# Kernel tuning notes

Hardware: AMD Instinct MI355X
Metric: run time of the kernel (lower is better)

The kernel has to match this reference:

```python
import jax, jax.numpy as jnp
import numpy as np

D, H, N, BS = 3072, 2048, 16, 512
MAX_LATENT_VAR = 0.1


def setup_inputs() -> dict:
    key = jax.random.key(0)
    ks = jax.random.split(key, 12)
    s = 0.02
    return {
        "x": jax.random.normal(ks[0], (BS, D), dtype=jnp.float32),
        "eps": jax.random.normal(ks[1], (1, BS, N), dtype=jnp.float32),
        "enc_W1": jax.random.normal(ks[2], (D, H), dtype=jnp.float32) * s,
        "enc_b1": jnp.zeros((H,), dtype=jnp.float32),
        "enc_Wmu": jax.random.normal(ks[3], (H, N), dtype=jnp.float32) * s,
        "enc_bmu": jnp.zeros((N,), dtype=jnp.float32),
        "enc_Wls": jax.random.normal(ks[4], (H, 1), dtype=jnp.float32) * s,
        "enc_bls": jnp.zeros((1,), dtype=jnp.float32),
        "dec_W1": jax.random.normal(ks[5], (N, H), dtype=jnp.float32) * 0.1,
        "dec_b1": jnp.zeros((H,), dtype=jnp.float32),
        "dec_W2": jax.random.normal(ks[6], (H, D), dtype=jnp.float32) * s,
        "dec_b2": jnp.zeros((D,), dtype=jnp.float32),
    }


def reference(x, eps, enc_W1, enc_b1, enc_Wmu, enc_bmu, enc_Wls, enc_bls,
              dec_W1, dec_b1, dec_W2, dec_b2):
    bs, Dd = x.shape
    n = dec_W1.shape[0]

    def dec(z):  # smooth 2-layer MLP decoder (supports nested autodiff)
        return jnp.tanh(z @ dec_W1 + dec_b1) @ dec_W2 + dec_b2

    # encoder.forward_with_sigma
    h = jnp.tanh(x @ enc_W1 + enc_b1)
    z_star = h @ enc_Wmu + enc_bmu                      # (bs, n)
    sigma = jnp.exp(h @ enc_Wls + enc_bls)[:, 0]        # (bs,)

    # per-sample Jacobian of decoder: (bs, D, n)
    J = jax.vmap(jax.jacfwd(dec))(z_star)

    # per-sample Hessian of f(z) = stop_grad(d) . d,  d = (x - dec(z)) / sigma
    def f_hess(z, xi, sg):
        d = (xi - dec(z)) / sg
        return jnp.dot(jax.lax.stop_gradient(d), d)
    hess = jax.vmap(jax.hessian(f_hess), in_axes=(0, 0, 0))(z_star, x, sigma)  # (bs,n,n)

    eye = jnp.eye(n, dtype=x.dtype)
    Prec = jnp.einsum('bdi,bdj->bij', J, J) / (sigma ** 2)[:, None, None] + eye + hess

    eigvals = jnp.linalg.eigvalsh(Prec)                 # ascending, (bs, n)
    eigmin = eigvals[:, 0]
    delta = 1.0 / MAX_LATENT_VAR - eigmin               # (bs,)
    Prec = Prec + eye * delta[:, None, None]
    eigvals = eigvals + delta[:, None]

    # upper-triangular Cholesky: U^T U = Prec
    U = jnp.swapaxes(jnp.linalg.cholesky(Prec), -1, -2)  # (bs, n, n)

    def solve1(u, e):  # solve U y = e
        return jax.scipy.linalg.solve_triangular(u, e[:, None], lower=False)[:, 0]
    z_off = jax.vmap(jax.vmap(solve1, in_axes=(0, 0)), in_axes=(None, 0))(U, eps)  # (ne,bs,n)
    z_sample = z_star[None] + z_off

    n_eval = eps.shape[0]
    recon = dec(z_sample.reshape(-1, n)).reshape(n_eval, bs, Dd)
    recon_loss = ((recon - x[None]) ** 2).sum(axis=2).mean(axis=0) / (2.0 * sigma ** 2)
    latent_energy = (z_star ** 2).sum(axis=1) / 2.0 + (1.0 / eigvals).sum(axis=1) / 2.0
    logdet_loss = jnp.log(eigvals).sum(axis=1) / 2.0
    sigma_loss = Dd * jnp.log(sigma)
    neg_log_prob = (recon_loss + latent_energy + logdet_loss + sigma_loss) / Dd
    return (neg_log_prob, recon_loss, latent_energy, logdet_loss, sigma)
```

## Files before the change

kernel.cpp:

```cpp
#include <hip/hip_runtime.h>
#include <hip/hip_bf16.h>
#include <math.h>

#define D_ 3072
#define H_ 2048
#define N_ 16
#define BS_ 512

typedef short s16x8 __attribute__((ext_vector_type(8)));
typedef float f32x4v __attribute__((ext_vector_type(4)));
typedef __hip_bfloat16 bf16;

__device__ __forceinline__ void gload_lds16(const void* g, void* l) {
    __builtin_amdgcn_global_load_lds((const __attribute__((address_space(1))) void*)g,
                                     (__attribute__((address_space(3))) void*)l, 16, 0, 0);
}

__device__ __forceinline__ float bf2f(unsigned short u) {
    unsigned v = (unsigned)u << 16; float f; __builtin_memcpy(&f, &v, 4); return f;
}

__global__ __launch_bounds__(256) void mfma_nt_slab(
    const bf16* __restrict__ A, const bf16* __restrict__ Bt,
    float* __restrict__ C, int M, int N, int K, int KC)
{
    __shared__ __align__(16) bf16 As[128 * 32];
    __shared__ __align__(16) bf16 Bs[128 * 32];
    const int tid = threadIdx.x;
    const int w = tid >> 6, l = tid & 63;
    const int wr = w >> 1, wc = w & 1;
    const int m0 = blockIdx.y * 128, n0 = blockIdx.x * 128;
    const int kbeg = blockIdx.z * KC;
    float* Cz = C + (size_t)blockIdx.z * M * N;

    f32x4v acc[4][4];
    #pragma unroll
    for (int a = 0; a < 4; ++a)
        #pragma unroll
        for (int b = 0; b < 4; ++b) acc[a][b] = (f32x4v){0.f, 0.f, 0.f, 0.f};

    const int srow = l >> 2;
    const int scol = (l & 3) * 8;

    for (int k0 = kbeg; k0 < kbeg + KC; k0 += 32) {
        #pragma unroll
        for (int q = 0; q < 2; ++q) {
            int r0 = w * 32 + q * 16;
            gload_lds16(&A[(size_t)(m0 + r0 + srow) * K + k0 + scol], &As[r0 * 32]);
            gload_lds16(&Bt[(size_t)(n0 + r0 + srow) * K + k0 + scol], &Bs[r0 * 32]);
        }
        __syncthreads();
        s16x8 af[4], bfr[4];
        #pragma unroll
        for (int mf = 0; mf < 4; ++mf)
            af[mf] = *(const s16x8*)&As[(wr * 64 + mf * 16 + (l & 15)) * 32 + (l >> 4) * 8];
        #pragma unroll
        for (int nf = 0; nf < 4; ++nf)
            bfr[nf] = *(const s16x8*)&Bs[(wc * 64 + nf * 16 + (l & 15)) * 32 + (l >> 4) * 8];
        #pragma unroll
        for (int mf = 0; mf < 4; ++mf)
            #pragma unroll
            for (int nf = 0; nf < 4; ++nf)
                acc[mf][nf] = __builtin_amdgcn_mfma_f32_16x16x32_bf16(af[mf], bfr[nf], acc[mf][nf], 0, 0, 0);
        __syncthreads();
    }

    #pragma unroll
    for (int mf = 0; mf < 4; ++mf)
        #pragma unroll
        for (int nf = 0; nf < 4; ++nf) {
            int n = n0 + wc * 64 + nf * 16 + (l & 15);
            #pragma unroll
            for (int r = 0; r < 4; ++r) {
                int m = m0 + wr * 64 + mf * 16 + (l >> 4) * 4 + r;
                Cz[(size_t)m * N + n] = acc[mf][nf][r];
            }
        }
}

__global__ __launch_bounds__(256) void mfma_nt_sk(
    const bf16* __restrict__ A, const bf16* __restrict__ Bt,
    float* __restrict__ C, int M, int N, int K, int KC)
{
    __shared__ __align__(16) bf16 As[128 * 32];
    __shared__ __align__(16) bf16 Bs[128 * 32];
    const int tid = threadIdx.x;
    const int w = tid >> 6, l = tid & 63;
    const int wr = w >> 1, wc = w & 1;
    const int m0 = blockIdx.y * 128, n0 = blockIdx.x * 128;
    const int kbeg = blockIdx.z * KC;

    f32x4v acc[4][4];
    #pragma unroll
    for (int a = 0; a < 4; ++a)
        #pragma unroll
        for (int b = 0; b < 4; ++b) acc[a][b] = (f32x4v){0.f, 0.f, 0.f, 0.f};

    const int srow = l >> 2;
    const int scol = (l & 3) * 8;

    for (int k0 = kbeg; k0 < kbeg + KC; k0 += 32) {
        #pragma unroll
        for (int q = 0; q < 2; ++q) {
            int r0 = w * 32 + q * 16;
            gload_lds16(&A[(size_t)(m0 + r0 + srow) * K + k0 + scol], &As[r0 * 32]);
            gload_lds16(&Bt[(size_t)(n0 + r0 + srow) * K + k0 + scol], &Bs[r0 * 32]);
        }
        __syncthreads();
        s16x8 af[4], bfr[4];
        #pragma unroll
        for (int mf = 0; mf < 4; ++mf)
            af[mf] = *(const s16x8*)&As[(wr * 64 + mf * 16 + (l & 15)) * 32 + (l >> 4) * 8];
        #pragma unroll
        for (int nf = 0; nf < 4; ++nf)
            bfr[nf] = *(const s16x8*)&Bs[(wc * 64 + nf * 16 + (l & 15)) * 32 + (l >> 4) * 8];
        #pragma unroll
        for (int mf = 0; mf < 4; ++mf)
            #pragma unroll
            for (int nf = 0; nf < 4; ++nf)
                acc[mf][nf] = __builtin_amdgcn_mfma_f32_16x16x32_bf16(af[mf], bfr[nf], acc[mf][nf], 0, 0, 0);
        __syncthreads();
    }

    #pragma unroll
    for (int mf = 0; mf < 4; ++mf)
        #pragma unroll
        for (int nf = 0; nf < 4; ++nf) {
            int n = n0 + wc * 64 + nf * 16 + (l & 15);
            #pragma unroll
            for (int r = 0; r < 4; ++r) {
                int m = m0 + wr * 64 + mf * 16 + (l >> 4) * 4 + r;
                atomicAdd(&C[(size_t)m * N + n], acc[mf][nf][r]);
            }
        }
}

__global__ __launch_bounds__(256) void ep_ebf(const float* __restrict__ C4,
    const float* __restrict__ bias, const float* __restrict__ X,
    bf16* __restrict__ Eout, int MN, int N)
{
    const size_t SL = (size_t)MN;
    int base = (blockIdx.x * 256 + threadIdx.x) * 8;
    if (base < MN) {
        float4 c0 = *(const float4*)&C4[base];
        float4 c1 = *(const float4*)&C4[base + 4];
        float4 d0 = *(const float4*)&C4[SL + base];
        float4 d1 = *(const float4*)&C4[SL + base + 4];
        float4 e0 = *(const float4*)&C4[2*SL + base];
        float4 e1 = *(const float4*)&C4[2*SL + base + 4];
        float4 f0 = *(const float4*)&C4[3*SL + base];
        float4 f1 = *(const float4*)&C4[3*SL + base + 4];
        float4 x0 = *(const float4*)&X[base];
        float4 x1 = *(const float4*)&X[base + 4];
        int n = base % N;
        float4 b0 = *(const float4*)&bias[n];
        float4 b1 = *(const float4*)&bias[n + 4];
        union { s16x8 v; bf16 e[8]; } u;
        u.e[0] = __float2bfloat16(x0.x - (c0.x + d0.x + e0.x + f0.x + b0.x));
        u.e[1] = __float2bfloat16(x0.y - (c0.y + d0.y + e0.y + f0.y + b0.y));
        u.e[2] = __float2bfloat16(x0.z - (c0.z + d0.z + e0.z + f0.z + b0.z));
        u.e[3] = __float2bfloat16(x0.w - (c0.w + d0.w + e0.w + f0.w + b0.w));
        u.e[4] = __float2bfloat16(x1.x - (c1.x + d1.x + e1.x + f1.x + b1.x));
        u.e[5] = __float2bfloat16(x1.y - (c1.y + d1.y + e1.y + f1.y + b1.y));
        u.e[6] = __float2bfloat16(x1.z - (c1.z + d1.z + e1.z + f1.z + b1.z));
        u.e[7] = __float2bfloat16(x1.w - (c1.w + d1.w + e1.w + f1.w + b1.w));
        *(s16x8*)&Eout[base] = u.v;
    }
}

__global__ __launch_bounds__(256) void ep_recon_fin(const float* __restrict__ C4,
    const float* __restrict__ bias, const float* __restrict__ X,
    const float* __restrict__ sigma, const float* __restrict__ lsig, float* __restrict__ d_out)
{
    const size_t SL = (size_t)BS_ * D_;
    int m = blockIdx.x;
    float s = 0.f;
    for (int n = threadIdx.x * 4; n < D_; n += 1024) {
        size_t i = (size_t)m * D_ + n;
        float4 c0 = *(const float4*)&C4[i];
        float4 c1 = *(const float4*)&C4[SL + i];
        float4 c2 = *(const float4*)&C4[2*SL + i];
        float4 c3 = *(const float4*)&C4[3*SL + i];
        float4 bb = *(const float4*)&bias[n];
        float4 xx = *(const float4*)&X[i];
        float v0 = c0.x + c1.x + c2.x + c3.x + bb.x - xx.x;
        float v1 = c0.y + c1.y + c2.y + c3.y + bb.y - xx.y;
        float v2 = c0.z + c1.z + c2.z + c3.z + bb.z - xx.z;
        float v3 = c0.w + c1.w + c2.w + c3.w + bb.w - xx.w;
        s += v0 * v0 + v1 * v1 + v2 * v2 + v3 * v3;
    }
    __shared__ float red[4];
    int wid = threadIdx.x >> 6, lane = threadIdx.x & 63;
    #pragma unroll
    for (int off = 32; off; off >>= 1) s += __shfl_xor(s, off);
    if (lane == 0) red[wid] = s;
    __syncthreads();
    if (threadIdx.x == 0) {
        float tot = red[0] + red[1] + red[2] + red[3];
        float sg = sigma[m];
        float rl = tot / (2.0f * sg * sg);
        float le = d_out[2 * 512 + m];
        float ld = d_out[3 * 512 + m];
        d_out[m] = (rl + le + ld) / 3072.0f + lsig[m];
        d_out[512 + m] = rl;
    }
}

__global__ __launch_bounds__(256) void jtj_fused(
    const bf16* __restrict__ Vt, const bf16* __restrict__ W2t,
    float* __restrict__ S, int Mb, int b0)
{
    __shared__ union {
        struct { __align__(16) bf16 As[3][128 * 32]; __align__(16) bf16 Bs[3][128 * 32]; } s;
        __align__(16) bf16 J[128 * 136];
    } u;
    const int tid = threadIdx.x;
    const int w = tid >> 6, l = tid & 63;
    const int wr = w >> 1, wc = w & 1;

    int mb, nbk;
    if ((Mb & 7) == 0) {
        int lin = blockIdx.y * 24 + blockIdx.x;
        int xcd = lin & 7, idx = lin >> 3;
        int mchunk = Mb >> 3;
        mb = xcd * mchunk + idx / 24;
        nbk = idx % 24;
    } else { mb = blockIdx.y; nbk = blockIdx.x; }
    const int m0 = mb * 128, n0 = nbk * 128;

    f32x4v acc[4][4];
    #pragma unroll
    for (int a = 0; a < 4; ++a)
        #pragma unroll
        for (int b = 0; b < 4; ++b) acc[a][b] = (f32x4v){0.f, 0.f, 0.f, 0.f};

    const int strow = tid >> 2;
    const int scb = (((tid & 3) ^ ((tid >> 3) & 3)) << 4);

    auto STAGE = [&](int kt, int bi) {
        const char* a0 = (const char*)Vt  + ((size_t)(m0 + strow) * H_ + kt * 32) * 2 + scb;
        const char* b0p = (const char*)W2t + ((size_t)(n0 + strow) * H_ + kt * 32) * 2 + scb;
        char* la = (char*)u.s.As[bi] + w * 1024;
        char* lb = (char*)u.s.Bs[bi] + w * 1024;
        gload_lds16(a0, la);
        gload_lds16(a0 + (size_t)64 * H_ * 2, la + 4096);
        gload_lds16(b0p, lb);
        gload_lds16(b0p + (size_t)64 * H_ * 2, lb + 4096);
    };

    STAGE(0, 0);
    STAGE(1, 1);

    const int rdcb = (((l >> 4) ^ ((l >> 1) & 3)) << 4);

    for (int kt = 0; kt < H_ / 32; ++kt) {
        __builtin_amdgcn_sched_barrier(0);
        if (kt == H_ / 32 - 1) asm volatile("s_waitcnt vmcnt(0)" ::: "memory");
        else                   asm volatile("s_waitcnt vmcnt(4)" ::: "memory");
        __builtin_amdgcn_s_barrier();
        __builtin_amdgcn_sched_barrier(0);
        const int cur = kt % 3;
        const char* Ab = (const char*)u.s.As[cur];
        const char* Bb = (const char*)u.s.Bs[cur];
        s16x8 af[4], bfr[4];
        #pragma unroll
        for (int mf = 0; mf < 4; ++mf)
            af[mf] = *(const s16x8*)(Ab + (wr * 64 + mf * 16 + (l & 15)) * 64 + rdcb);
        #pragma unroll
        for (int nf = 0; nf < 4; ++nf)
            bfr[nf] = *(const s16x8*)(Bb + (wc * 64 + nf * 16 + (l & 15)) * 64 + rdcb);
        if (kt + 2 < H_ / 32) STAGE(kt + 2, (kt + 2) % 3);
        #pragma unroll
        for (int mf = 0; mf < 4; ++mf)
            #pragma unroll
            for (int nf = 0; nf < 4; ++nf)
                acc[mf][nf] = __builtin_amdgcn_mfma_f32_16x16x32_bf16(af[mf], bfr[nf], acc[mf][nf], 0, 0, 0);
    }

    __syncthreads();
    #pragma unroll
    for (int mf = 0; mf < 4; ++mf) {
        int rbase = wr * 64 + mf * 16 + (l >> 4) * 4;
        #pragma unroll
        for (int nf = 0; nf < 4; ++nf) {
            int col = wc * 64 + nf * 16 + (l & 15);
            #pragma unroll
            for (int r = 0; r < 4; ++r)
                u.J[(rbase + r) * 136 + col] = __float2bfloat16(acc[mf][nf][r]);
        }
    }
    __syncthreads();

    #pragma unroll
    for (int t2 = 0; t2 < 2; ++t2) {
        int bl = w * 2 + t2;
        f32x4v sp = (f32x4v){0.f, 0.f, 0.f, 0.f};
        #pragma unroll
        for (int kq = 0; kq < 4; ++kq) {
            s16x8 fr = *(const s16x8*)&u.J[(bl * 16 + (l & 15)) * 136 + kq * 32 + (l >> 4) * 8];
            sp = __builtin_amdgcn_mfma_f32_16x16x32_bf16(fr, fr, sp, 0, 0, 0);
        }
        int bglob = b0 + mb * 8 + bl;
        #pragma unroll
        for (int r = 0; r < 4; ++r)
            atomicAdd(&S[(size_t)bglob * 256 + ((l >> 4) * 4 + r) * 16 + (l & 15)], sp[r]);
    }
}

__global__ __launch_bounds__(256) void hess_mfma(const float* __restrict__ t,
    const float* __restrict__ g, const bf16* __restrict__ W1b, float* __restrict__ S)
{
    const int w = threadIdx.x >> 6, l = threadIdx.x & 63;
    const int b = blockIdx.x * 4 + w;
    const int row = l & 15, kq = (l >> 4) * 8;

    f32x4v sp = (f32x4v){0.f, 0.f, 0.f, 0.f};
    for (int k0 = 0; k0 < H_; k0 += 32) {
        int kk = k0 + kq;
        s16x8 wf = *(const s16x8*)&W1b[(size_t)row * H_ + kk];
        float4 t0 = *(const float4*)&t[(size_t)b * H_ + kk];
        float4 t1 = *(const float4*)&t[(size_t)b * H_ + kk + 4];
        float4 g0 = *(const float4*)&g[(size_t)b * H_ + kk];
        float4 g1 = *(const float4*)&g[(size_t)b * H_ + kk + 4];
        float wv[8];
        wv[0] = 2.f * g0.x * t0.x * (1.f - t0.x * t0.x);
        wv[1] = 2.f * g0.y * t0.y * (1.f - t0.y * t0.y);
        wv[2] = 2.f * g0.z * t0.z * (1.f - t0.z * t0.z);
        wv[3] = 2.f * g0.w * t0.w * (1.f - t0.w * t0.w);
        wv[4] = 2.f * g1.x * t1.x * (1.f - t1.x * t1.x);
        wv[5] = 2.f * g1.y * t1.y * (1.f - t1.y * t1.y);
        wv[6] = 2.f * g1.z * t1.z * (1.f - t1.z * t1.z);
        wv[7] = 2.f * g1.w * t1.w * (1.f - t1.w * t1.w);
        union { s16x8 v; bf16 e[8]; } af;
        #pragma unroll
        for (int e = 0; e < 8; ++e)
            af.e[e] = __float2bfloat16(wv[e] * bf2f((unsigned short)wf[e]));
        sp = __builtin_amdgcn_mfma_f32_16x16x32_bf16(af.v, wf, sp, 0, 0, 0);
    }
    #pragma unroll
    for (int r = 0; r < 4; ++r)
        S[(size_t)b * 256 + ((l >> 4) * 4 + r) * 16 + (l & 15)] += sp[r];
}

__global__ __launch_bounds__(256) void prep_all(
    const float* __restrict__ x, const float* __restrict__ enc_W1,
    const float* __restrict__ dec_W2, const float* __restrict__ dec_W1,
    bf16* __restrict__ x_bf, bf16* __restrict__ eW1t,
    bf16* __restrict__ W2t, bf16* __restrict__ W2b, bf16* __restrict__ W1b)
{
    __shared__ float tile[64][65];
    const int blk = blockIdx.x;
    const int tid = threadIdx.x;
    if (blk < 768) {
        int i = blk * 256 + tid;
        const float4* p = (const float4*)x + (size_t)i * 2;
        float4 a = p[0], b = p[1];
        union { s16x8 v; bf16 e[8]; } u;
        u.e[0] = __float2bfloat16(a.x); u.e[1] = __float2bfloat16(a.y);
        u.e[2] = __float2bfloat16(a.z); u.e[3] = __float2bfloat16(a.w);
        u.e[4] = __float2bfloat16(b.x); u.e[5] = __float2bfloat16(b.y);
        u.e[6] = __float2bfloat16(b.z); u.e[7] = __float2bfloat16(b.w);
        *(s16x8*)&x_bf[(size_t)i * 8] = u.v;
    } else if (blk < 768 + 1536) {
        int bid = blk - 768;
        int r0 = (bid % 48) * 64, c0 = (bid / 48) * 64;
        int tx = tid & 63, ty = tid >> 6;
        #pragma unroll
        for (int k = 0; k < 16; ++k) {
            int rr = ty * 16 + k;
            tile[rr][tx] = enc_W1[(size_t)(r0 + rr) * H_ + c0 + tx];
        }
        __syncthreads();
        #pragma unroll
        for (int k = 0; k < 16; ++k) {
            int cc = ty * 16 + k;
            eW1t[(size_t)(c0 + cc) * D_ + r0 + tx] = __float2bfloat16(tile[tx][cc]);
        }
    } else if (blk < 768 + 3072) {
        int bid = blk - 768 - 1536;
        int r0 = (bid % 32) * 64, c0 = (bid / 32) * 64;
        int tx = tid & 63, ty = tid >> 6;
        #pragma unroll
        for (int k = 0; k < 16; ++k) {
            int rr = ty * 16 + k;
            float v = dec_W2[(size_t)(r0 + rr) * D_ + c0 + tx];
            tile[rr][tx] = v;
            W2b[(size_t)(r0 + rr) * D_ + c0 + tx] = __float2bfloat16(v);
        }
        __syncthreads();
        #pragma unroll
        for (int k = 0; k < 16; ++k) {
            int cc = ty * 16 + k;
            W2t[(size_t)(c0 + cc) * H_ + r0 + tx] = __float2bfloat16(tile[tx][cc]);
        }
    } else {
        int i = (blk - 768 - 3072) * 256 + tid;
        if (i < N_ * H_ / 8) {
            const float4* p = (const float4*)dec_W1 + (size_t)i * 2;
            float4 a = p[0], b = p[1];
            union { s16x8 v; bf16 e[8]; } u;
            u.e[0] = __float2bfloat16(a.x); u.e[1] = __float2bfloat16(a.y);
            u.e[2] = __float2bfloat16(a.z); u.e[3] = __float2bfloat16(a.w);
            u.e[4] = __float2bfloat16(b.x); u.e[5] = __float2bfloat16(b.y);
            u.e[6] = __float2bfloat16(b.z); u.e[7] = __float2bfloat16(b.w);
            *(s16x8*)&W1b[(size_t)i * 8] = u.v;
        }
    }
}

__global__ __launch_bounds__(256) void zsig_t_kernel(const float* __restrict__ Ch4,
    const float* __restrict__ enc_b1, const float* __restrict__ Wmu, const float* __restrict__ bmu,
    const float* __restrict__ Wls, const float* __restrict__ bls,
    const float* __restrict__ dW1, const float* __restrict__ db1,
    float* __restrict__ z_star, float* __restrict__ lsig, float* __restrict__ sigma,
    float* __restrict__ t, bf16* __restrict__ tb, bf16* __restrict__ Vt)
{
    const int b = blockIdx.x, tid = threadIdx.x;
    const size_t SL = (size_t)BS_ * H_;
    float acc[17];
    #pragma unroll
    for (int i = 0; i < 17; ++i) acc[i] = 0.f;
    for (int hh = tid; hh < H_; hh += 256) {
        size_t idx = (size_t)b * H_ + hh;
        float c = Ch4[idx] + Ch4[SL + idx] + Ch4[2*SL + idx] + Ch4[3*SL + idx];
        float hv = tanhf(c + enc_b1[hh]);
        const float* wr = &Wmu[(size_t)hh * 16];
        #pragma unroll
        for (int i = 0; i < 16; ++i) acc[i] += hv * wr[i];
        acc[16] += hv * Wls[hh];
    }
    __shared__ float red[17][4];
    __shared__ float zs[16];
    __shared__ float us[H_];
    const int wid = tid >> 6, lane = tid & 63;
    #pragma unroll
    for (int i = 0; i < 17; ++i) {
        float v = acc[i];
        #pragma unroll
        for (int off = 32; off; off >>= 1) v += __shfl_xor(v, off);
        if (lane == 0) red[i][wid] = v;
    }
    __syncthreads();
    if (tid < 17) {
        float v = red[tid][0] + red[tid][1] + red[tid][2] + red[tid][3];
        if (tid < 16) { float z = v + bmu[tid]; zs[tid] = z; z_star[(size_t)b * 16 + tid] = z; }
        else { float ls = v + bls[0]; lsig[b] = ls; sigma[b] = expf(ls); }
    }
    __syncthreads();
    for (int hh = tid; hh < H_; hh += 256) {
        float a = db1[hh];
        #pragma unroll
        for (int i = 0; i < 16; ++i) a += zs[i] * dW1[(size_t)i * H_ + hh];
        float tv = tanhf(a);
        t[(size_t)b * H_ + hh] = tv;
        tb[(size_t)b * H_ + hh] = __float2bfloat16(tv);
        us[hh] = 1.f - tv * tv;
    }
    if (Vt) {
        __syncthreads();
        size_t base = (size_t)b * 16 * H_;
        int hh = tid * 8;
        for (int i = 0; i < 16; ++i) {
            union { s16x8 v; bf16 e[8]; } pk;
            #pragma unroll
            for (int k = 0; k < 8; ++k)
                pk.e[k] = __float2bfloat16(us[hh + k] * dW1[(size_t)i * H_ + hh + k]);
            *(s16x8*)&Vt[base + (size_t)i * H_ + hh] = pk.v;
        }
    }
}

__global__ __launch_bounds__(256) void build_t(const float* __restrict__ z,
    const float* __restrict__ W1, const float* __restrict__ b1, bf16* __restrict__ tb)
{
    __shared__ float zs[16];
    int b = blockIdx.x, tid = threadIdx.x;
    if (tid < 16) zs[tid] = z[(size_t)b * 16 + tid];
    __syncthreads();
    for (int hh = tid; hh < H_; hh += 256) {
        float a = b1[hh];
        #pragma unroll
        for (int i = 0; i < 16; ++i) a += zs[i] * W1[(size_t)i * H_ + hh];
        tb[(size_t)b * H_ + hh] = __float2bfloat16(tanhf(a));
    }
}

__global__ __launch_bounds__(256) void build_vt(const float* __restrict__ t,
    const float* __restrict__ W1, bf16* __restrict__ Vt, int b0)
{
    int bl = blockIdx.x, b = b0 + bl, tid = threadIdx.x;
    __shared__ float u[H_];
    for (int hh = tid; hh < H_; hh += 256) {
        float tv = t[(size_t)b * H_ + hh];
        u[hh] = 1.f - tv * tv;
    }
    __syncthreads();
    size_t base = (size_t)bl * 16 * H_;
    int hh = tid * 8;
    for (int i = 0; i < 16; ++i) {
        union { s16x8 v; bf16 e[8]; } pk;
        #pragma unroll
        for (int k = 0; k < 8; ++k)
            pk.e[k] = __float2bfloat16(u[hh + k] * W1[(size_t)i * H_ + hh + k]);
        *(s16x8*)&Vt[base + (size_t)i * H_ + hh] = pk.v;
    }
}

__global__ __launch_bounds__(64) void solve_kernel(const float* __restrict__ S,
    const float* __restrict__ sigma, const float* __restrict__ z_star,
    const float* __restrict__ eps, float* __restrict__ z_sample, float* __restrict__ d_out)
{
    const int lane = threadIdx.x;
    const int q = lane >> 4;
    const int j = lane & 15;
    const int b = blockIdx.x * 4 + q;

    const float sg = sigma[b];
    const float inv_s2 = 1.0f / (sg * sg);

    float a0[16], a[16];
    #pragma unroll
    for (int r = 0; r < 16; ++r) {
        a0[r] = S[(size_t)b * 256 + r * 16 + j] * inv_s2 + ((r == j) ? 1.0f : 0.0f);
        a[r] = a0[r];
    }

    #pragma unroll
    for (int k = 0; k < 14; ++k) {
        float x[16];
        #pragma unroll
        for (int r = 0; r < 16; ++r) x[r] = __shfl(a[k], r, 16);
        float sig2 = 0.f;
        #pragma unroll
        for (int r = 0; r < 16; ++r) if (r > k + 1) sig2 += x[r] * x[r];
        float x0 = x[k + 1];
        float normx = sqrtf(sig2 + x0 * x0);
        float alpha = (x0 >= 0.f) ? -normx : normx;
        float v[16];
        #pragma unroll
        for (int r = 0; r < 16; ++r)
            v[r] = (r <= k) ? 0.f : ((r == k + 1) ? x0 - alpha : x[r]);
        float vtv = 0.f;
        #pragma unroll
        for (int r = 0; r < 16; ++r) vtv += v[r] * v[r];
        float beta = (vtv > 1e-28f) ? 2.0f / vtv : 0.f;
        float sj = 0.f;
        #pragma unroll
        for (int r = 0; r < 16; ++r) sj += a[r] * v[r];
        float av[16];
        #pragma unroll
        for (int r = 0; r < 16; ++r) av[r] = __shfl(sj, r, 16);
        float vtav = 0.f;
        #pragma unroll
        for (int r = 0; r < 16; ++r) vtav += v[r] * av[r];
        float c = 0.5f * beta * vtav;
        float wv[16];
        #pragma unroll
        for (int r = 0; r < 16; ++r) wv[r] = beta * (av[r] - c * v[r]);
        float vj = (j <= k) ? 0.f : ((j == k + 1) ? a[k] - alpha : a[k]);
        float wj = beta * (sj - c * vj);
        #pragma unroll
        for (int r = 0; r < 16; ++r) a[r] -= v[r] * wj + wv[r] * vj;
    }

    float dg[16], eo[15];
    #pragma unroll
    for (int r = 0; r < 16; ++r) dg[r] = __shfl(a[r], r, 16);
    #pragma unroll
    for (int r = 0; r < 15; ++r) eo[r] = __shfl(a[r + 1], r, 16);

    float lo = 1e30f, hi = 1e30f;
    #pragma unroll
    for (int r = 0; r < 16; ++r) {
        float rad = ((r > 0) ? fabsf(eo[r - 1]) : 0.f) + ((r < 15) ? fabsf(eo[r]) : 0.f);
        lo = fminf(lo, dg[r] - rad);
        hi = fminf(hi, dg[r]);
    }
    lo -= 1e-4f; hi += 1e-4f;

    #pragma unroll
    for (int pass = 0; pass < 5; ++pass) {
        float step = (hi - lo) * (1.0f / 17.0f);
        float s = lo + step * (float)(j + 1);
        float qq = dg[0] - s;
        int cnt = (qq < 0.f) ? 1 : 0;
        #pragma unroll
        for (int i = 1; i < 16; ++i) {
            float denom = (fabsf(qq) < 1e-30f) ? -1e-30f : qq;
            qq = dg[i] - s - eo[i - 1] * eo[i - 1] / denom;
            cnt += (qq < 0.f) ? 1 : 0;
        }
        unsigned long long bal = __ballot(cnt >= 1);
        unsigned grp = (unsigned)((bal >> (q * 16)) & 0xffffull);
        int f = grp ? (__ffs(grp) - 1) : 16;
        float nlo = lo + step * (float)f;
        float nhi = (f < 16) ? (lo + step * (float)(f + 1)) : hi;
        lo = nlo; hi = nhi;
    }
    const float lam_min = 0.5f * (lo + hi);
    const float delta = 10.0f - lam_min;

    float bm[16];
    #pragma unroll
    for (int r = 0; r < 16; ++r) bm[r] = a0[r] + ((r == j) ? delta : 0.f);

    float ldsum = 0.f;
    #pragma unroll
    for (int kk = 0; kk < 16; ++kk) {
        float ck[16];
        #pragma unroll
        for (int r = 0; r < 16; ++r) ck[r] = __shfl(bm[kk], r, 16);
        float dkk = sqrtf(fmaxf(ck[kk], 1e-30f));
        float inv = 1.0f / dkk;
        ldsum += logf(dkk);
        float lfull[16];
        #pragma unroll
        for (int r = 0; r < 16; ++r) lfull[r] = ck[r] * inv;
        float lj = bm[kk] * inv;
        if (j == kk) {
            #pragma unroll
            for (int r = 0; r < 16; ++r) bm[r] = (r >= kk) ? lfull[r] : 0.f;
        } else if (j > kk) {
            #pragma unroll
            for (int r = 0; r < 16; ++r)
                if (r > kk) bm[r] -= lfull[r] * lj;
        }
    }

    float w[16];
    #pragma unroll
    for (int r = 0; r < 16; ++r) w[r] = 0.f;
    #pragma unroll
    for (int i = 0; i < 16; ++i) {
        float row[16];
        #pragma unroll
        for (int kx = 0; kx < 16; ++kx) row[kx] = __shfl(bm[i], kx, 16);
        float sacc = 0.f;
        #pragma unroll
        for (int kx = 0; kx < 16; ++kx) if (kx < i) sacc += row[kx] * w[kx];
        float invd = 1.0f / row[i];
        float val = (i == j) ? invd : (-sacc * invd);
        w[i] = (i >= j) ? val : 0.f;
    }

    float tsum = 0.f;
    #pragma unroll
    for (int r = 0; r < 16; ++r) tsum += w[r] * w[r];
    float zv = z_star[(size_t)b * 16 + j];
    float ep = eps[(size_t)b * 16 + j];
    float epsv[16];
    #pragma unroll
    for (int r = 0; r < 16; ++r) epsv[r] = __shfl(ep, r, 16);
    float zoff = 0.f;
    #pragma unroll
    for (int r = 0; r < 16; ++r) zoff += w[r] * epsv[r];
    z_sample[(size_t)b * 16 + j] = zv + zoff;

    float zsq = zv * zv;
    #pragma unroll
    for (int off = 1; off < 16; off <<= 1) {
        tsum += __shfl_xor(tsum, off);
        zsq  += __shfl_xor(zsq, off);
    }
    if (j == 0) {
        d_out[2 * 512 + b] = 0.5f * zsq + 0.5f * tsum;
        d_out[3 * 512 + b] = ldsum;
        d_out[4 * 512 + b] = sg;
    }
}

extern "C" void kernel_launch(void* const* d_in, const int* in_sizes, int n_in,
                              void* d_out, int out_size, void* d_ws, size_t ws_size,
                              hipStream_t stream)
{
    const float* x       = (const float*)d_in[0];
    const float* eps     = (const float*)d_in[1];
    const float* enc_W1  = (const float*)d_in[2];
    const float* enc_b1  = (const float*)d_in[3];
    const float* enc_Wmu = (const float*)d_in[4];
    const float* enc_bmu = (const float*)d_in[5];
    const float* enc_Wls = (const float*)d_in[6];
    const float* enc_bls = (const float*)d_in[7];
    const float* dec_W1  = (const float*)d_in[8];
    const float* dec_b1  = (const float*)d_in[9];
    const float* dec_W2  = (const float*)d_in[10];
    const float* dec_b2  = (const float*)d_in[11];
    float* out = (float*)d_out;

    char* wsb = (char*)d_ws;
    size_t off = 0;
    auto alloc = [&](size_t bytes) -> void* {
        off = (off + 255) & ~(size_t)255;
        void* p = wsb + off;
        off += bytes;
        return p;
    };

    float* g    = (float*)alloc((size_t)BS_ * H_ * 4);
    float* S    = (float*)alloc((size_t)BS_ * 256 * 4);
    size_t zero_span = (size_t)((char*)(S + BS_ * 256) - (char*)g);

    float* Ch4  = (float*)alloc((size_t)4 * BS_ * H_ * 4);
    float* Cd4  = (float*)alloc((size_t)4 * BS_ * D_ * 4);
    float* t    = (float*)alloc((size_t)BS_ * H_ * 4);
    float* z_st = (float*)alloc((size_t)BS_ * 16 * 4);
    float* lsig = (float*)alloc(BS_ * 4);
    float* sigm = (float*)alloc(BS_ * 4);
    float* z_sm = (float*)alloc((size_t)BS_ * 16 * 4);
    bf16* x_bf  = (bf16*)alloc((size_t)BS_ * D_ * 2);
    bf16* eW1t  = (bf16*)alloc((size_t)H_ * D_ * 2);
    bf16* W2b   = (bf16*)alloc((size_t)H_ * D_ * 2);
    bf16* W2t   = (bf16*)alloc((size_t)D_ * H_ * 2);
    bf16* W1b   = (bf16*)alloc((size_t)N_ * H_ * 2);
    bf16* t_bf  = (bf16*)alloc((size_t)BS_ * H_ * 2);
    bf16* e_bf  = (bf16*)alloc((size_t)BS_ * D_ * 2);
    bf16* t2b   = (bf16*)alloc((size_t)BS_ * H_ * 2);

    int nb = 0;
    size_t base_off = off;
    const int cand[3] = {512, 128, 32};
    bf16* Vt = nullptr;
    for (int ci = 0; ci < 3; ++ci) {
        off = base_off;
        int n = cand[ci];
        bf16* vt = (bf16*)alloc((size_t)n * 16 * H_ * 2);
        if (off <= ws_size) { nb = n; Vt = vt; break; }
    }
    if (nb == 0) return;
    bf16* Vt_full = (nb == 512) ? Vt : nullptr;

    prep_all<<<dim3(768 + 3072 + 16), 256, 0, stream>>>(
        x, enc_W1, dec_W2, dec_W1, x_bf, eW1t, W2t, W2b, W1b);
    hipMemsetAsync(g, 0, zero_span, stream);

    mfma_nt_slab<<<dim3(H_ / 128, BS_ / 128, 4), 256, 0, stream>>>(
        x_bf, eW1t, Ch4, BS_, H_, D_, D_ / 4);
    zsig_t_kernel<<<dim3(BS_), 256, 0, stream>>>(Ch4, enc_b1, enc_Wmu, enc_bmu, enc_Wls, enc_bls,
        dec_W1, dec_b1, z_st, lsig, sigm, t, t_bf, Vt_full);
    mfma_nt_slab<<<dim3(D_ / 128, BS_ / 128, 4), 256, 0, stream>>>(
        t_bf, W2t, Cd4, BS_, D_, H_, H_ / 4);
    ep_ebf<<<dim3(BS_ * D_ / 8 / 256), 256, 0, stream>>>(Cd4, dec_b2, x, e_bf, BS_ * D_, D_);
    mfma_nt_sk<<<dim3(H_ / 128, BS_ / 128, 4), 256, 0, stream>>>(
        e_bf, W2b, g, BS_, H_, D_, D_ / 4);

    if (Vt_full) {
        jtj_fused<<<dim3(D_ / 128, 512 * 16 / 128), 256, 0, stream>>>(
            Vt_full, W2t, S, 512 * 16 / 128, 0);
    } else {
        for (int b0 = 0; b0 < BS_; b0 += nb) {
            build_vt<<<dim3(nb), 256, 0, stream>>>(t, dec_W1, Vt, b0);
            jtj_fused<<<dim3(D_ / 128, nb * 16 / 128), 256, 0, stream>>>(
                Vt, W2t, S, nb * 16 / 128, b0);
        }
    }
    hess_mfma<<<dim3(BS_ / 4), 256, 0, stream>>>(t, g, W1b, S);

    solve_kernel<<<dim3(BS_ / 4), 64, 0, stream>>>(S, sigm, z_st, eps, z_sm, out);
    build_t<<<dim3(BS_), 256, 0, stream>>>(z_sm, dec_W1, dec_b1, t2b);
    mfma_nt_slab<<<dim3(D_ / 128, BS_ / 128, 4), 256, 0, stream>>>(
        t2b, W2t, Cd4, BS_, D_, H_, H_ / 4);
    ep_recon_fin<<<dim3(BS_), 256, 0, stream>>>(Cd4, dec_b2, x, sigm, lsig, out);
}
```

Before: 322.1 us.

## Use eight split-K slabs, fuse Hessian into solve, fold memset into prep

Raises the split-K factor of the slab GEMMs from 4 to 8 to put more blocks on the device, and widens the slab-summing epilogues to match. The Hessian MFMA kernel is merged into the solve kernel: it writes to shared memory and is added to S at load time, which removes a launch and a global read-modify-write of S. The hipMemsetAsync of g and S is replaced by extra zeroing blocks inside prep_all. The cost is twice the fp32 partial-slab memory, more slab traffic in the epilogues, and three of the four waves sitting idle during the solve phase.

```diff
diff --git a/kernel.cpp b/kernel.cpp
--- a/kernel.cpp
+++ b/kernel.cpp
@@ -6,6 +6,7 @@
 #define H_ 2048
 #define N_ 16
 #define BS_ 512
+#define NSL_ 8
 
 typedef short s16x8 __attribute__((ext_vector_type(8)));
 typedef float f32x4v __attribute__((ext_vector_type(4)));
@@ -135,40 +136,40 @@
         }
 }
 
-__global__ __launch_bounds__(256) void ep_ebf(const float* __restrict__ C4,
+__global__ __launch_bounds__(256) void ep_ebf(const float* __restrict__ C8,
     const float* __restrict__ bias, const float* __restrict__ X,
     bf16* __restrict__ Eout, int MN, int N)
 {
     const size_t SL = (size_t)MN;
     int base = (blockIdx.x * 256 + threadIdx.x) * 8;
     if (base < MN) {
-        float4 c0 = *(const float4*)&C4[base];
-        float4 c1 = *(const float4*)&C4[base + 4];
-        float4 d0 = *(const float4*)&C4[SL + base];
-        float4 d1 = *(const float4*)&C4[SL + base + 4];
-        float4 e0 = *(const float4*)&C4[2*SL + base];
-        float4 e1 = *(const float4*)&C4[2*SL + base + 4];
-        float4 f0 = *(const float4*)&C4[3*SL + base];
-        float4 f1 = *(const float4*)&C4[3*SL + base + 4];
+        float v[8] = {0.f, 0.f, 0.f, 0.f, 0.f, 0.f, 0.f, 0.f};
+        #pragma unroll
+        for (int s = 0; s < NSL_; ++s) {
+            float4 c0 = *(const float4*)&C8[s * SL + base];
+            float4 c1 = *(const float4*)&C8[s * SL + base + 4];
+            v[0] += c0.x; v[1] += c0.y; v[2] += c0.z; v[3] += c0.w;
+            v[4] += c1.x; v[5] += c1.y; v[6] += c1.z; v[7] += c1.w;
+        }
         float4 x0 = *(const float4*)&X[base];
         float4 x1 = *(const float4*)&X[base + 4];
         int n = base % N;
         float4 b0 = *(const float4*)&bias[n];
         float4 b1 = *(const float4*)&bias[n + 4];
-        union { s16x8 v; bf16 e[8]; } u;
-        u.e[0] = __float2bfloat16(x0.x - (c0.x + d0.x + e0.x + f0.x + b0.x));
-        u.e[1] = __float2bfloat16(x0.y - (c0.y + d0.y + e0.y + f0.y + b0.y));
-        u.e[2] = __float2bfloat16(x0.z - (c0.z + d0.z + e0.z + f0.z + b0.z));
-        u.e[3] = __float2bfloat16(x0.w - (c0.w + d0.w + e0.w + f0.w + b0.w));
-        u.e[4] = __float2bfloat16(x1.x - (c1.x + d1.x + e1.x + f1.x + b1.x));
-        u.e[5] = __float2bfloat16(x1.y - (c1.y + d1.y + e1.y + f1.y + b1.y));
-        u.e[6] = __float2bfloat16(x1.z - (c1.z + d1.z + e1.z + f1.z + b1.z));
-        u.e[7] = __float2bfloat16(x1.w - (c1.w + d1.w + e1.w + f1.w + b1.w));
-        *(s16x8*)&Eout[base] = u.v;
-    }
-}
-
-__global__ __launch_bounds__(256) void ep_recon_fin(const float* __restrict__ C4,
+        union { s16x8 vv; bf16 e[8]; } u;
+        u.e[0] = __float2bfloat16(x0.x - (v[0] + b0.x));
+        u.e[1] = __float2bfloat16(x0.y - (v[1] + b0.y));
+        u.e[2] = __float2bfloat16(x0.z - (v[2] + b0.z));
+        u.e[3] = __float2bfloat16(x0.w - (v[3] + b0.w));
+        u.e[4] = __float2bfloat16(x1.x - (v[4] + b1.x));
+        u.e[5] = __float2bfloat16(x1.y - (v[5] + b1.y));
+        u.e[6] = __float2bfloat16(x1.z - (v[6] + b1.z));
+        u.e[7] = __float2bfloat16(x1.w - (v[7] + b1.w));
+        *(s16x8*)&Eout[base] = u.vv;
+    }
+}
+
+__global__ __launch_bounds__(256) void ep_recon_fin(const float* __restrict__ C8,
     const float* __restrict__ bias, const float* __restrict__ X,
     const float* __restrict__ sigma, const float* __restrict__ lsig, float* __restrict__ d_out)
 {
@@ -177,16 +178,18 @@
     float s = 0.f;
     for (int n = threadIdx.x * 4; n < D_; n += 1024) {
         size_t i = (size_t)m * D_ + n;
-        float4 c0 = *(const float4*)&C4[i];
-        float4 c1 = *(const float4*)&C4[SL + i];
-        float4 c2 = *(const float4*)&C4[2*SL + i];
-        float4 c3 = *(const float4*)&C4[3*SL + i];
+        float4 acc4 = (float4){0.f, 0.f, 0.f, 0.f};
+        #pragma unroll
+        for (int sl = 0; sl < NSL_; ++sl) {
+            float4 c = *(const float4*)&C8[sl * SL + i];
+            acc4.x += c.x; acc4.y += c.y; acc4.z += c.z; acc4.w += c.w;
+        }
         float4 bb = *(const float4*)&bias[n];
         float4 xx = *(const float4*)&X[i];
-        float v0 = c0.x + c1.x + c2.x + c3.x + bb.x - xx.x;
-        float v1 = c0.y + c1.y + c2.y + c3.y + bb.y - xx.y;
-        float v2 = c0.z + c1.z + c2.z + c3.z + bb.z - xx.z;
-        float v3 = c0.w + c1.w + c2.w + c3.w + bb.w - xx.w;
+        float v0 = acc4.x + bb.x - xx.x;
+        float v1 = acc4.y + bb.y - xx.y;
+        float v2 = acc4.z + bb.z - xx.z;
+        float v3 = acc4.w + bb.w - xx.w;
         s += v0 * v0 + v1 * v1 + v2 * v2 + v3 * v3;
     }
     __shared__ float red[4];
@@ -307,46 +310,12 @@
     }
 }
 
-__global__ __launch_bounds__(256) void hess_mfma(const float* __restrict__ t,
-    const float* __restrict__ g, const bf16* __restrict__ W1b, float* __restrict__ S)
-{
-    const int w = threadIdx.x >> 6, l = threadIdx.x & 63;
-    const int b = blockIdx.x * 4 + w;
-    const int row = l & 15, kq = (l >> 4) * 8;
-
-    f32x4v sp = (f32x4v){0.f, 0.f, 0.f, 0.f};
-    for (int k0 = 0; k0 < H_; k0 += 32) {
-        int kk = k0 + kq;
-        s16x8 wf = *(const s16x8*)&W1b[(size_t)row * H_ + kk];
-        float4 t0 = *(const float4*)&t[(size_t)b * H_ + kk];
-        float4 t1 = *(const float4*)&t[(size_t)b * H_ + kk + 4];
-        float4 g0 = *(const float4*)&g[(size_t)b * H_ + kk];
-        float4 g1 = *(const float4*)&g[(size_t)b * H_ + kk + 4];
-        float wv[8];
-        wv[0] = 2.f * g0.x * t0.x * (1.f - t0.x * t0.x);
-        wv[1] = 2.f * g0.y * t0.y * (1.f - t0.y * t0.y);
-        wv[2] = 2.f * g0.z * t0.z * (1.f - t0.z * t0.z);
-        wv[3] = 2.f * g0.w * t0.w * (1.f - t0.w * t0.w);
-        wv[4] = 2.f * g1.x * t1.x * (1.f - t1.x * t1.x);
-        wv[5] = 2.f * g1.y * t1.y * (1.f - t1.y * t1.y);
-        wv[6] = 2.f * g1.z * t1.z * (1.f - t1.z * t1.z);
-        wv[7] = 2.f * g1.w * t1.w * (1.f - t1.w * t1.w);
-        union { s16x8 v; bf16 e[8]; } af;
-        #pragma unroll
-        for (int e = 0; e < 8; ++e)
-            af.e[e] = __float2bfloat16(wv[e] * bf2f((unsigned short)wf[e]));
-        sp = __builtin_amdgcn_mfma_f32_16x16x32_bf16(af.v, wf, sp, 0, 0, 0);
-    }
-    #pragma unroll
-    for (int r = 0; r < 4; ++r)
-        S[(size_t)b * 256 + ((l >> 4) * 4 + r) * 16 + (l & 15)] += sp[r];
-}
-
 __global__ __launch_bounds__(256) void prep_all(
     const float* __restrict__ x, const float* __restrict__ enc_W1,
     const float* __restrict__ dec_W2, const float* __restrict__ dec_W1,
     bf16* __restrict__ x_bf, bf16* __restrict__ eW1t,
-    bf16* __restrict__ W2t, bf16* __restrict__ W2b, bf16* __restrict__ W1b)
+    bf16* __restrict__ W2t, bf16* __restrict__ W2b, bf16* __restrict__ W1b,
+    float* __restrict__ zero_region)
 {
     __shared__ float tile[64][65];
     const int blk = blockIdx.x;
@@ -393,7 +362,7 @@
             int cc = ty * 16 + k;
             W2t[(size_t)(c0 + cc) * H_ + r0 + tx] = __float2bfloat16(tile[tx][cc]);
         }
-    } else {
+    } else if (blk < 768 + 3072 + 16) {
         int i = (blk - 768 - 3072) * 256 + tid;
         if (i < N_ * H_ / 8) {
             const float4* p = (const float4*)dec_W1 + (size_t)i * 2;
@@ -405,10 +374,13 @@
             u.e[6] = __float2bfloat16(b.z); u.e[7] = __float2bfloat16(b.w);
             *(s16x8*)&W1b[(size_t)i * 8] = u.v;
         }
-    }
-}
-
-__global__ __launch_bounds__(256) void zsig_t_kernel(const float* __restrict__ Ch4,
+    } else {
+        int i = (blk - 768 - 3072 - 16) * 256 + tid;
+        *(float4*)&zero_region[(size_t)i * 4] = (float4){0.f, 0.f, 0.f, 0.f};
+    }
+}
+
+__global__ __launch_bounds__(256) void zsig_t_kernel(const float* __restrict__ Ch8,
     const float* __restrict__ enc_b1, const float* __restrict__ Wmu, const float* __restrict__ bmu,
     const float* __restrict__ Wls, const float* __restrict__ bls,
     const float* __restrict__ dW1, const float* __restrict__ db1,
@@ -422,7 +394,9 @@
     for (int i = 0; i < 17; ++i) acc[i] = 0.f;
     for (int hh = tid; hh < H_; hh += 256) {
         size_t idx = (size_t)b * H_ + hh;
-        float c = Ch4[idx] + Ch4[SL + idx] + Ch4[2*SL + idx] + Ch4[3*SL + idx];
+        float c = 0.f;
+        #pragma unroll
+        for (int s = 0; s < NSL_; ++s) c += Ch8[s * SL + idx];
         float hv = tanhf(c + enc_b1[hh]);
         const float* wr = &Wmu[(size_t)hh * 16];
         #pragma unroll
@@ -506,11 +480,49 @@
     }
 }
 
-__global__ __launch_bounds__(64) void solve_kernel(const float* __restrict__ S,
-    const float* __restrict__ sigma, const float* __restrict__ z_star,
-    const float* __restrict__ eps, float* __restrict__ z_sample, float* __restrict__ d_out)
-{
-    const int lane = threadIdx.x;
+__global__ __launch_bounds__(256) void solve_hess_kernel(
+    const float* __restrict__ S, const float* __restrict__ t, const float* __restrict__ g,
+    const bf16* __restrict__ W1b, const float* __restrict__ sigma,
+    const float* __restrict__ z_star, const float* __restrict__ eps,
+    float* __restrict__ z_sample, float* __restrict__ d_out)
+{
+    __shared__ float Sh[4][256];
+    const int tid = threadIdx.x;
+    {
+        const int w = tid >> 6, l = tid & 63;
+        const int b = blockIdx.x * 4 + w;
+        const int row = l & 15, kq = (l >> 4) * 8;
+        f32x4v sp = (f32x4v){0.f, 0.f, 0.f, 0.f};
+        for (int k0 = 0; k0 < H_; k0 += 32) {
+            int kk = k0 + kq;
+            s16x8 wf = *(const s16x8*)&W1b[(size_t)row * H_ + kk];
+            float4 t0 = *(const float4*)&t[(size_t)b * H_ + kk];
+            float4 t1 = *(const float4*)&t[(size_t)b * H_ + kk + 4];
+            float4 g0 = *(const float4*)&g[(size_t)b * H_ + kk];
+            float4 g1 = *(const float4*)&g[(size_t)b * H_ + kk + 4];
+            float wv[8];
+            wv[0] = 2.f * g0.x * t0.x * (1.f - t0.x * t0.x);
+            wv[1] = 2.f * g0.y * t0.y * (1.f - t0.y * t0.y);
+            wv[2] = 2.f * g0.z * t0.z * (1.f - t0.z * t0.z);
+            wv[3] = 2.f * g0.w * t0.w * (1.f - t0.w * t0.w);
+            wv[4] = 2.f * g1.x * t1.x * (1.f - t1.x * t1.x);
+            wv[5] = 2.f * g1.y * t1.y * (1.f - t1.y * t1.y);
+            wv[6] = 2.f * g1.z * t1.z * (1.f - t1.z * t1.z);
+            wv[7] = 2.f * g1.w * t1.w * (1.f - t1.w * t1.w);
+            union { s16x8 v; bf16 e[8]; } af;
+            #pragma unroll
+            for (int e = 0; e < 8; ++e)
+                af.e[e] = __float2bfloat16(wv[e] * bf2f((unsigned short)wf[e]));
+            sp = __builtin_amdgcn_mfma_f32_16x16x32_bf16(af.v, wf, sp, 0, 0, 0);
+        }
+        #pragma unroll
+        for (int r = 0; r < 4; ++r)
+            Sh[w][((l >> 4) * 4 + r) * 16 + (l & 15)] = sp[r];
+    }
+    __syncthreads();
+    if (tid >= 64) return;
+
+    const int lane = tid;
     const int q = lane >> 4;
     const int j = lane & 15;
     const int b = blockIdx.x * 4 + q;
@@ -521,7 +533,7 @@
     float a0[16], a[16];
     #pragma unroll
     for (int r = 0; r < 16; ++r) {
-        a0[r] = S[(size_t)b * 256 + r * 16 + j] * inv_s2 + ((r == j) ? 1.0f : 0.0f);
+        a0[r] = (S[(size_t)b * 256 + r * 16 + j] + Sh[q][r * 16 + j]) * inv_s2 + ((r == j) ? 1.0f : 0.0f);
         a[r] = a0[r];
     }
 
@@ -698,10 +710,9 @@
 
     float* g    = (float*)alloc((size_t)BS_ * H_ * 4);
     float* S    = (float*)alloc((size_t)BS_ * 256 * 4);
-    size_t zero_span = (size_t)((char*)(S + BS_ * 256) - (char*)g);
-
-    float* Ch4  = (float*)alloc((size_t)4 * BS_ * H_ * 4);
-    float* Cd4  = (float*)alloc((size_t)4 * BS_ * D_ * 4);
+
+    float* Ch8  = (float*)alloc((size_t)NSL_ * BS_ * H_ * 4);
+    float* Cd8  = (float*)alloc((size_t)NSL_ * BS_ * D_ * 4);
     float* t    = (float*)alloc((size_t)BS_ * H_ * 4);
     float* z_st = (float*)alloc((size_t)BS_ * 16 * 4);
     float* lsig = (float*)alloc(BS_ * 4);
@@ -729,17 +740,16 @@
     if (nb == 0) return;
     bf16* Vt_full = (nb == 512) ? Vt : nullptr;
 
-    prep_all<<<dim3(768 + 3072 + 16), 256, 0, stream>>>(
-        x, enc_W1, dec_W2, dec_W1, x_bf, eW1t, W2t, W2b, W1b);
-    hipMemsetAsync(g, 0, zero_span, stream);
-
-    mfma_nt_slab<<<dim3(H_ / 128, BS_ / 128, 4), 256, 0, stream>>>(
-        x_bf, eW1t, Ch4, BS_, H_, D_, D_ / 4);
-    zsig_t_kernel<<<dim3(BS_), 256, 0, stream>>>(Ch4, enc_b1, enc_Wmu, enc_bmu, enc_Wls, enc_bls,
+    prep_all<<<dim3(768 + 3072 + 16 + 1152), 256, 0, stream>>>(
+        x, enc_W1, dec_W2, dec_W1, x_bf, eW1t, W2t, W2b, W1b, g);
+
+    mfma_nt_slab<<<dim3(H_ / 128, BS_ / 128, NSL_), 256, 0, stream>>>(
+        x_bf, eW1t, Ch8, BS_, H_, D_, D_ / NSL_);
+    zsig_t_kernel<<<dim3(BS_), 256, 0, stream>>>(Ch8, enc_b1, enc_Wmu, enc_bmu, enc_Wls, enc_bls,
         dec_W1, dec_b1, z_st, lsig, sigm, t, t_bf, Vt_full);
-    mfma_nt_slab<<<dim3(D_ / 128, BS_ / 128, 4), 256, 0, stream>>>(
-        t_bf, W2t, Cd4, BS_, D_, H_, H_ / 4);
-    ep_ebf<<<dim3(BS_ * D_ / 8 / 256), 256, 0, stream>>>(Cd4, dec_b2, x, e_bf, BS_ * D_, D_);
+    mfma_nt_slab<<<dim3(D_ / 128, BS_ / 128, NSL_), 256, 0, stream>>>(
+        t_bf, W2t, Cd8, BS_, D_, H_, H_ / NSL_);
+    ep_ebf<<<dim3(BS_ * D_ / 8 / 256), 256, 0, stream>>>(Cd8, dec_b2, x, e_bf, BS_ * D_, D_);
     mfma_nt_sk<<<dim3(H_ / 128, BS_ / 128, 4), 256, 0, stream>>>(
         e_bf, W2b, g, BS_, H_, D_, D_ / 4);
 
@@ -753,11 +763,11 @@
                 Vt, W2t, S, nb * 16 / 128, b0);
         }
     }
-    hess_mfma<<<dim3(BS_ / 4), 256, 0, stream>>>(t, g, W1b, S);
-
-    solve_kernel<<<dim3(BS_ / 4), 64, 0, stream>>>(S, sigm, z_st, eps, z_sm, out);
+
+    solve_hess_kernel<<<dim3(BS_ / 4), 256, 0, stream>>>(
+        S, t, g, W1b, sigm, z_st, eps, z_sm, out);
     build_t<<<dim3(BS_), 256, 0, stream>>>(z_sm, dec_W1, dec_b1, t2b);
-    mfma_nt_slab<<<dim3(D_ / 128, BS_ / 128, 4), 256, 0, stream>>>(
-        t2b, W2t, Cd4, BS_, D_, H_, H_ / 4);
-    ep_recon_fin<<<dim3(BS_), 256, 0, stream>>>(Cd4, dec_b2, x, sigm, lsig, out);
-}
+    mfma_nt_slab<<<dim3(D_ / 128, BS_ / 128, NSL_), 256, 0, stream>>>(
+        t2b, W2t, Cd8, BS_, D_, H_, H_ / NSL_);
+    ep_recon_fin<<<dim3(BS_), 256, 0, stream>>>(Cd8, dec_b2, x, sigm, lsig, out);
+}
```

Result: faster. 310.6 us (median of 3 runs) (-3.6%).
